# Performance work log

Measured on AMD Instinct MI355X. Metric: run time of the kernel, lower is better.

## Reference

```python
import jax, jax.numpy as jnp
import numpy as np
import math

QUERY_SIZE = 128
KEY_SIZE = 128
VALUE_SIZE = 64
ATTN_SIZE = 64
NQ = 4096
NK = 8192


def setup_inputs() -> dict:
    key = jax.random.key(0)
    ks = jax.random.split(key, 9)
    scale_q = 1.0 / math.sqrt(QUERY_SIZE)
    scale_k = 1.0 / math.sqrt(KEY_SIZE)
    scale_v = 1.0 / math.sqrt(VALUE_SIZE)
    return {
        "q": jax.random.normal(ks[0], (NQ, QUERY_SIZE), jnp.float32),
        "k": jax.random.normal(ks[1], (NK, KEY_SIZE), jnp.float32),
        "v": jax.random.normal(ks[2], (NK, VALUE_SIZE), jnp.float32),
        # nn.Linear weights: [out_features, in_features], y = x W^T + b
        "Wq": jax.random.uniform(ks[3], (ATTN_SIZE, QUERY_SIZE), jnp.float32, -scale_q, scale_q),
        "bq": jax.random.uniform(ks[4], (ATTN_SIZE,), jnp.float32, -scale_q, scale_q),
        "Wk": jax.random.uniform(ks[5], (ATTN_SIZE, KEY_SIZE), jnp.float32, -scale_k, scale_k),
        "bk": jax.random.uniform(ks[6], (ATTN_SIZE,), jnp.float32, -scale_k, scale_k),
        "Wv": jax.random.uniform(ks[7], (VALUE_SIZE, VALUE_SIZE), jnp.float32, -scale_v, scale_v),
        "bv": jax.random.uniform(ks[8], (VALUE_SIZE,), jnp.float32, -scale_v, scale_v),
    }


def reference(q, k, v, Wq, bq, Wk, bk, Wv, bv):
    # Linear projections (y = x W^T + b)
    query = q @ Wq.T + bq          # [Nq, A]
    key_p = k @ Wk.T + bk          # [Nk, A]
    value = v @ Wv.T + bv          # [Nk, Dv]
    # scaled dot-product scores
    g = (query @ key_p.T) / math.sqrt(ATTN_SIZE)   # [Nq, Nk]
    score = jax.nn.softmax(g, axis=-1)
    # sum(score[...,None] * value, axis=-2) == score @ value
    output = score @ value          # [Nq, Dv]
    return output
```

## Files before the change

### kernel.cpp

```cpp
#include <hip/hip_runtime.h>
#include <hip/hip_bf16.h>

typedef __bf16 bf16;
typedef __bf16 bf16x4 __attribute__((ext_vector_type(4)));
typedef __bf16 bf16x8 __attribute__((ext_vector_type(8)));
typedef float floatx4 __attribute__((ext_vector_type(4)));

#define MFMA16(A, B, C) __builtin_amdgcn_mfma_f32_16x16x32_bf16(A, B, C, 0, 0, 0)

constexpr int NQ = 4096;
constexpr int NK = 8192;
constexpr int AD = 64;
constexpr int KSPLIT = 32;
constexpr int BQ = 128;
constexpr int BK = 64;
constexpr int KPB = NK / KSPLIT;
constexpr int TILES = KPB / BK;
constexpr float QSCALE = 0.125f * 1.4426950408889634f;

__device__ inline bf16x8 ld_cvt8(const float* __restrict__ p) {
  float4 a = *(const float4*)p;
  float4 b = *(const float4*)(p + 4);
  bf16x8 r = {(bf16)a.x, (bf16)a.y, (bf16)a.z, (bf16)a.w,
              (bf16)b.x, (bf16)b.y, (bf16)b.z, (bf16)b.w};
  return r;
}

__global__ __launch_bounds__(256) void proj_mfma(
    const float* __restrict__ q, const float* __restrict__ k,
    const float* __restrict__ v,
    const float* __restrict__ Wq, const float* __restrict__ bq,
    const float* __restrict__ Wk, const float* __restrict__ bk,
    const float* __restrict__ Wv, const float* __restrict__ bv,
    bf16* __restrict__ qout, bf16* __restrict__ kout, bf16* __restrict__ vtout) {
  const int tid = threadIdx.x;
  const int wave = tid >> 6, lane = tid & 63;
  const int l16 = lane & 15, quad = lane >> 4;
  const int b = blockIdx.x;

  if (b < 192) {
    const bool isQ = (b < 64);
    const float* X = isQ ? q : k;
    const float* W = isQ ? Wq : Wk;
    const float* bias = isQ ? bq : bk;
    bf16* Y = isQ ? qout : kout;
    const float oscale = isQ ? QSCALE : 1.0f;
    const int rowbase = (isQ ? b : b - 64) * 64 + wave * 16;

    bf16x8 bf_[4];
#pragma unroll
    for (int ks = 0; ks < 4; ++ks)
      bf_[ks] = ld_cvt8(X + (size_t)(rowbase + l16) * 128 + ks * 32 + quad * 8);
    bf16x8 af[4][4];
#pragma unroll
    for (int mt = 0; mt < 4; ++mt)
#pragma unroll
      for (int ks = 0; ks < 4; ++ks)
        af[mt][ks] = ld_cvt8(W + (size_t)(mt * 16 + l16) * 128 + ks * 32 + quad * 8);

    floatx4 acc[4];
#pragma unroll
    for (int mt = 0; mt < 4; ++mt) acc[mt] = (floatx4){0.f, 0.f, 0.f, 0.f};
#pragma unroll
    for (int mt = 0; mt < 4; ++mt)
#pragma unroll
      for (int ks = 0; ks < 4; ++ks)
        acc[mt] = MFMA16(af[mt][ks], bf_[ks], acc[mt]);

#pragma unroll
    for (int mt = 0; mt < 4; ++mt) {
      float4 bb = *(const float4*)(bias + mt * 16 + quad * 4);
      bf16x4 o = {(bf16)((acc[mt][0] + bb.x) * oscale),
                  (bf16)((acc[mt][1] + bb.y) * oscale),
                  (bf16)((acc[mt][2] + bb.z) * oscale),
                  (bf16)((acc[mt][3] + bb.w) * oscale)};
      *(bf16x4*)(Y + (size_t)(rowbase + l16) * 64 + mt * 16 + quad * 4) = o;
    }
  } else {
    const int keybase = (b - 192) * 64 + wave * 16;
    bf16x8 af2[2];
#pragma unroll
    for (int ks = 0; ks < 2; ++ks)
      af2[ks] = ld_cvt8(v + (size_t)(keybase + l16) * 64 + ks * 32 + quad * 8);
    bf16x8 bf2[4][2];
#pragma unroll
    for (int nt = 0; nt < 4; ++nt)
#pragma unroll
      for (int ks = 0; ks < 2; ++ks)
        bf2[nt][ks] = ld_cvt8(Wv + (size_t)(nt * 16 + l16) * 64 + ks * 32 + quad * 8);

    floatx4 acc[4];
#pragma unroll
    for (int nt = 0; nt < 4; ++nt) acc[nt] = (floatx4){0.f, 0.f, 0.f, 0.f};
#pragma unroll
    for (int nt = 0; nt < 4; ++nt)
#pragma unroll
      for (int ks = 0; ks < 2; ++ks)
        acc[nt] = MFMA16(af2[ks], bf2[nt][ks], acc[nt]);

#pragma unroll
    for (int nt = 0; nt < 4; ++nt) {
      float bvv = bv[nt * 16 + l16];
      bf16x4 o = {(bf16)(acc[nt][0] + bvv), (bf16)(acc[nt][1] + bvv),
                  (bf16)(acc[nt][2] + bvv), (bf16)(acc[nt][3] + bvv)};
      *(bf16x4*)(vtout + (size_t)(nt * 16 + l16) * NK + keybase + quad * 4) = o;
    }
  }
}

__global__ __launch_bounds__(256, 4) void flash_kernel(
    const bf16* __restrict__ qp, const bf16* __restrict__ kp,
    const bf16* __restrict__ vt, bf16* __restrict__ Opart,
    float* __restrict__ lpart) {
  __shared__ __align__(16) bf16 Kt[BK][64];
  __shared__ __align__(16) bf16 Vts[AD][64];
  __shared__ __align__(16) bf16 Pt[4][32][64];

  const int tid = threadIdx.x;
  const int wave = tid >> 6;
  const int lane = tid & 63;
  const int l16 = lane & 15;
  const int quad = lane >> 4;
  const int h = l16 & 7;
  const int ks = blockIdx.x;
  const int qb = blockIdx.y;
  const int qbase = qb * BQ + wave * 32;

  const int srow = tid >> 3, scg = tid & 7;
  const int sswz = (scg ^ (srow & 7)) * 8;

  bf16x8 qf[2][2];
#pragma unroll
  for (int g = 0; g < 2; ++g)
#pragma unroll
    for (int c = 0; c < 2; ++c)
      qf[g][c] = *(const bf16x8*)(qp + (size_t)(qbase + g * 16 + l16) * AD +
                                  c * 32 + quad * 8);

  floatx4 o[2][4];
#pragma unroll
  for (int g = 0; g < 2; ++g)
#pragma unroll
    for (int nt = 0; nt < 4; ++nt)
      o[g][nt] = (floatx4){0.f, 0.f, 0.f, 0.f};
  float lsum[2] = {0.f, 0.f};

  int kb0 = ks * KPB;
  bf16x8 kpre0 = *(const bf16x8*)(kp + (size_t)(kb0 + srow) * AD + scg * 8);
  bf16x8 kpre1 = *(const bf16x8*)(kp + (size_t)(kb0 + srow + 32) * AD + scg * 8);
  bf16x8 vpre0 = *(const bf16x8*)(vt + (size_t)srow * NK + kb0 + scg * 8);
  bf16x8 vpre1 = *(const bf16x8*)(vt + (size_t)(srow + 32) * NK + kb0 + scg * 8);

#pragma unroll
  for (int kt = 0; kt < TILES; ++kt) {
    const int nb = ks * KPB + ((kt + 1) & (TILES - 1)) * BK;

    __syncthreads();
    *(bf16x8*)&Kt[srow][sswz] = kpre0;
    *(bf16x8*)&Kt[srow + 32][sswz] = kpre1;
    *(bf16x8*)&Vts[srow][sswz] = vpre0;
    *(bf16x8*)&Vts[srow + 32][sswz] = vpre1;
    __syncthreads();

    kpre0 = *(const bf16x8*)(kp + (size_t)(nb + srow) * AD + scg * 8);
    kpre1 = *(const bf16x8*)(kp + (size_t)(nb + srow + 32) * AD + scg * 8);

#pragma unroll
    for (int st = 0; st < 4; ++st) {
      bf16x8 ka0 = *(const bf16x8*)&Kt[st * 16 + l16][(quad ^ h) * 8];
      bf16x8 ka1 = *(const bf16x8*)&Kt[st * 16 + l16][((quad + 4) ^ h) * 8];
#pragma unroll
      for (int g = 0; g < 2; ++g) {
        floatx4 acc = {0.f, 0.f, 0.f, 0.f};
        acc = MFMA16(ka0, qf[g][0], acc);
        acc = MFMA16(ka1, qf[g][1], acc);
        float p0 = __builtin_amdgcn_exp2f(acc[0]);
        float p1 = __builtin_amdgcn_exp2f(acc[1]);
        float p2 = __builtin_amdgcn_exp2f(acc[2]);
        float p3 = __builtin_amdgcn_exp2f(acc[3]);
        lsum[g] += (p0 + p1) + (p2 + p3);
        bf16x4 pk = {(bf16)p0, (bf16)p1, (bf16)p2, (bf16)p3};
        int pcol = ((st * 2 + (quad >> 1)) ^ h) * 8 + (quad & 1) * 4;
        *(bf16x4*)&Pt[wave][g * 16 + l16][pcol] = pk;
      }
    }

    vpre0 = *(const bf16x8*)(vt + (size_t)srow * NK + nb + scg * 8);
    vpre1 = *(const bf16x8*)(vt + (size_t)(srow + 32) * NK + nb + scg * 8);

    bf16x8 pf[2][2];
#pragma unroll
    for (int g = 0; g < 2; ++g)
#pragma unroll
      for (int c = 0; c < 2; ++c)
        pf[g][c] =
            *(const bf16x8*)&Pt[wave][g * 16 + l16][((quad + c * 4) ^ h) * 8];

#pragma unroll
    for (int nt = 0; nt < 4; ++nt) {
      bf16x8 vb0 = *(const bf16x8*)&Vts[nt * 16 + l16][(quad ^ h) * 8];
      bf16x8 vb1 = *(const bf16x8*)&Vts[nt * 16 + l16][((quad + 4) ^ h) * 8];
#pragma unroll
      for (int g = 0; g < 2; ++g) {
        o[g][nt] = MFMA16(pf[g][0], vb0, o[g][nt]);
        o[g][nt] = MFMA16(pf[g][1], vb1, o[g][nt]);
      }
    }
  }

#pragma unroll
  for (int g = 0; g < 2; ++g) {
    float t = lsum[g];
    t += __shfl_xor(t, 16, 64);
    t += __shfl_xor(t, 32, 64);
    lsum[g] = t;
  }

  bf16* ob = Opart + (size_t)ks * NQ * AD + (size_t)qbase * AD;
#pragma unroll
  for (int g = 0; g < 2; ++g)
#pragma unroll
    for (int nt = 0; nt < 4; ++nt)
#pragma unroll
      for (int r = 0; r < 4; ++r)
        ob[(size_t)(g * 16 + quad * 4 + r) * AD + nt * 16 + l16] =
            (bf16)o[g][nt][r];
  if (quad == 0) {
#pragma unroll
    for (int g = 0; g < 2; ++g)
      lpart[(size_t)ks * NQ + qbase + g * 16 + l16] = lsum[g];
  }
}

__global__ __launch_bounds__(256) void combine_kernel(
    const bf16* __restrict__ Opart, const float* __restrict__ lpart,
    float* __restrict__ out) {
  int t = blockIdx.x * 256 + threadIdx.x;
  int gid = t * 4;
  int qrow = gid >> 6;
  float ls = 0.f;
#pragma unroll
  for (int s = 0; s < KSPLIT; ++s) ls += lpart[(size_t)s * NQ + qrow];
  float a0 = 0.f, a1 = 0.f, a2 = 0.f, a3 = 0.f;
#pragma unroll
  for (int s = 0; s < KSPLIT; ++s) {
    bf16x4 ov = *(const bf16x4*)(Opart + (size_t)s * NQ * AD + gid);
    a0 += (float)ov[0];
    a1 += (float)ov[1];
    a2 += (float)ov[2];
    a3 += (float)ov[3];
  }
  float inv = 1.0f / ls;
  float4 res = {a0 * inv, a1 * inv, a2 * inv, a3 * inv};
  *(float4*)(out + gid) = res;
}

extern "C" void kernel_launch(void* const* d_in, const int* in_sizes, int n_in,
                              void* d_out, int out_size, void* d_ws,
                              size_t ws_size, hipStream_t stream) {
  const float* q = (const float*)d_in[0];
  const float* k = (const float*)d_in[1];
  const float* v = (const float*)d_in[2];
  const float* Wq = (const float*)d_in[3];
  const float* bq = (const float*)d_in[4];
  const float* Wk = (const float*)d_in[5];
  const float* bk = (const float*)d_in[6];
  const float* Wv = (const float*)d_in[7];
  const float* bv = (const float*)d_in[8];
  float* out = (float*)d_out;

  char* ws = (char*)d_ws;
  bf16* qout = (bf16*)(ws);
  bf16* kout = (bf16*)(ws + 524288);
  bf16* vtout = (bf16*)(ws + 1572864);
  bf16* Opart = (bf16*)(ws + 2621440);
  float* lpart = (float*)(ws + 2621440 + (size_t)KSPLIT * NQ * AD * 2);

  proj_mfma<<<320, 256, 0, stream>>>(q, k, v, Wq, bq, Wk, bk, Wv, bv, qout,
                                     kout, vtout);
  flash_kernel<<<dim3(KSPLIT, NQ / BQ), 256, 0, stream>>>(qout, kout, vtout,
                                                          Opart, lpart);
  flash_kernel<<<dim3(KSPLIT, NQ / BQ), 256, 0, stream>>>(qout, kout, vtout,
                                                          Opart, lpart);
  combine_kernel<<<NQ * AD / 1024, 256, 0, stream>>>(Opart, lpart, out);
}
```

Measured before the change: 116.7 us.

## Accumulate split-K flash partials with atomics and drop duplicate flash launch

The flash kernel now atomically adds its fp32 partial outputs and row sums into a zeroed global accumulator instead of writing per-split bf16 partials. The combine kernel becomes a simple normalize pass. The redundant second flash launch is removed. This trades partial-buffer traffic and a reduction kernel for 8M global atomics plus a memset, and results become order-nondeterministic.

```diff
diff --git a/kernel.cpp b/kernel.cpp
--- a/kernel.cpp
+++ b/kernel.cpp
@@ -110,8 +110,8 @@
 
 __global__ __launch_bounds__(256, 4) void flash_kernel(
     const bf16* __restrict__ qp, const bf16* __restrict__ kp,
-    const bf16* __restrict__ vt, bf16* __restrict__ Opart,
-    float* __restrict__ lpart) {
+    const bf16* __restrict__ vt, float* __restrict__ Oacc,
+    float* __restrict__ lacc) {
   __shared__ __align__(16) bf16 Kt[BK][64];
   __shared__ __align__(16) bf16 Vts[AD][64];
   __shared__ __align__(16) bf16 Pt[4][32][64];
@@ -216,42 +216,31 @@
     lsum[g] = t;
   }
 
-  bf16* ob = Opart + (size_t)ks * NQ * AD + (size_t)qbase * AD;
+  float* oa = Oacc + (size_t)qbase * AD;
 #pragma unroll
   for (int g = 0; g < 2; ++g)
 #pragma unroll
     for (int nt = 0; nt < 4; ++nt)
 #pragma unroll
       for (int r = 0; r < 4; ++r)
-        ob[(size_t)(g * 16 + quad * 4 + r) * AD + nt * 16 + l16] =
-            (bf16)o[g][nt][r];
+        atomicAdd(oa + (size_t)(g * 16 + quad * 4 + r) * AD + nt * 16 + l16,
+                  o[g][nt][r]);
   if (quad == 0) {
 #pragma unroll
     for (int g = 0; g < 2; ++g)
-      lpart[(size_t)ks * NQ + qbase + g * 16 + l16] = lsum[g];
-  }
-}
-
-__global__ __launch_bounds__(256) void combine_kernel(
-    const bf16* __restrict__ Opart, const float* __restrict__ lpart,
+      atomicAdd(lacc + qbase + g * 16 + l16, lsum[g]);
+  }
+}
+
+__global__ __launch_bounds__(256) void normalize_kernel(
+    const float* __restrict__ Oacc, const float* __restrict__ lacc,
     float* __restrict__ out) {
   int t = blockIdx.x * 256 + threadIdx.x;
   int gid = t * 4;
   int qrow = gid >> 6;
-  float ls = 0.f;
-#pragma unroll
-  for (int s = 0; s < KSPLIT; ++s) ls += lpart[(size_t)s * NQ + qrow];
-  float a0 = 0.f, a1 = 0.f, a2 = 0.f, a3 = 0.f;
-#pragma unroll
-  for (int s = 0; s < KSPLIT; ++s) {
-    bf16x4 ov = *(const bf16x4*)(Opart + (size_t)s * NQ * AD + gid);
-    a0 += (float)ov[0];
-    a1 += (float)ov[1];
-    a2 += (float)ov[2];
-    a3 += (float)ov[3];
-  }
-  float inv = 1.0f / ls;
-  float4 res = {a0 * inv, a1 * inv, a2 * inv, a3 * inv};
+  float inv = 1.0f / lacc[qrow];
+  float4 a = *(const float4*)(Oacc + gid);
+  float4 res = {a.x * inv, a.y * inv, a.z * inv, a.w * inv};
   *(float4*)(out + gid) = res;
 }
 
@@ -270,17 +259,17 @@
   float* out = (float*)d_out;
 
   char* ws = (char*)d_ws;
-  bf16* qout = (bf16*)(ws);
-  bf16* kout = (bf16*)(ws + 524288);
-  bf16* vtout = (bf16*)(ws + 1572864);
-  bf16* Opart = (bf16*)(ws + 2621440);
-  float* lpart = (float*)(ws + 2621440 + (size_t)KSPLIT * NQ * AD * 2);
+  float* Oacc = (float*)(ws);
+  float* lacc = (float*)(ws + 1048576);
+  bf16* qout = (bf16*)(ws + 1064960);
+  bf16* kout = (bf16*)(ws + 1589248);
+  bf16* vtout = (bf16*)(ws + 2637824);
+
+  hipMemsetAsync(Oacc, 0, 1064960, stream);
 
   proj_mfma<<<320, 256, 0, stream>>>(q, k, v, Wq, bq, Wk, bk, Wv, bv, qout,
                                      kout, vtout);
   flash_kernel<<<dim3(KSPLIT, NQ / BQ), 256, 0, stream>>>(qout, kout, vtout,
-                                                          Opart, lpart);
-  flash_kernel<<<dim3(KSPLIT, NQ / BQ), 256, 0, stream>>>(qout, kout, vtout,
-                                                          Opart, lpart);
-  combine_kernel<<<NQ * AD / 1024, 256, 0, stream>>>(Opart, lpart, out);
-}
+                                                          Oacc, lacc);
+  normalize_kernel<<<NQ * AD / 1024, 256, 0, stream>>>(Oacc, lacc, out);
+}
```

Result: slower. 120.2 us (+3.0%).
